# Optimization experiments

Measured on AMD Instinct MI355X. Metric: run time of the kernel, lower is better.

Reference implementation:

```python
import jax, jax.numpy as jnp
import numpy as np

MAX_LEN = 30
CONST_VAL = 0.0

def setup_inputs() -> dict:
    key = jax.random.key(0)
    k1, k2, k3 = jax.random.split(key, 3)
    B, T, F = 131072, 30, 10
    inputs = jax.random.normal(k1, (B, T, F), dtype=jnp.float32)
    w1 = jax.random.normal(k2, (1, MAX_LEN), dtype=jnp.float32) * 0.05
    w2 = jax.random.normal(k3, (1, MAX_LEN), dtype=jnp.float32) * 0.05
    return {"inputs": inputs, "w1": w1, "w2": w2}

def reference(inputs, w1, w2):
    B, T, F = inputs.shape  # T == 30 (hardcoded split count), F < MAX_LEN
    # matmul of (B,1,1) scalar with (1,max_len) == outer product -> (B, max_len)
    r1 = inputs[:, 0, 0][:, None] * w1[0]  # (B, 30)
    r2 = inputs[:, 0, 1][:, None] * w2[0]  # (B, 30)
    # concat along last dim then flatten rows, matching tf concat+reshape(-1,2)
    rc = jnp.stack([r1, r2], axis=-1).reshape(-1, 2)  # (N, 2), N = B*30
    N = rc.shape[0]
    K = (MAX_LEN - F) // 2  # number of shifted copies (original + K-1 shifts)
    # pad K-1 constant rows on top; shift i is rows [K-1-i : K-1-i+N] of padded
    pad = jnp.full((K - 1, 2), CONST_VAL, dtype=jnp.float32)
    P = jnp.concatenate([pad, rc], axis=0)  # (N+K-1, 2)
    shifts = jnp.stack(
        [jax.lax.dynamic_slice_in_dim(P, K - 1 - i, N, axis=0) for i in range(K)],
        axis=1,
    )  # (N, K, 2); shift-major column order matches tf.concat axis=1 order
    tens = shifts.reshape(N, 2 * K)  # (N, 2K)
    # tf.split(30, axis=0) + stack(axis=1): piece j row a = tens[j*B + a]
    tens = tens.reshape(30, B, 2 * K).transpose(1, 0, 2)  # (B, 30, 2K)
    return jnp.concatenate([tens, inputs[:, :, 2:]], axis=2)  # (B, 30, 2K+F-2)
```

## Files before the change

### kernel.cpp

```cpp
#include <hip/hip_runtime.h>


__global__ __launch_bounds__(256) void assign_kernel(
    const float* __restrict__ inp,
    const float* __restrict__ w1,
    const float* __restrict__ w2,
    float* __restrict__ out,
    int B, int nrows) {
    __shared__ float w1s[32], w2s[32];
    int t = threadIdx.x;
    if (t < 30) w1s[t] = w1[t];
    else if (t >= 32 && t < 62) w2s[t - 32] = w2[t - 32];
    __syncthreads();

    int row = blockIdx.x * blockDim.x + t;
    if (row >= nrows) return;

    int b = row / 30;
    int j = row - b * 30;
    int m0 = j * B + b;
    int q0 = m0 / 30;
    int r0 = m0 - q0 * 30;

    float2 xa = *(const float2*)(inp + (size_t)q0 * 300);
    float2 xb = (q0 >= 1) ? *(const float2*)(inp + (size_t)(q0 - 1) * 300)
                          : make_float2(0.f, 0.f);

    float front[20];
#pragma unroll
    for (int i = 0; i < 10; ++i) {
        bool useA = (r0 >= i);
        float2 x = useA ? xa : xb;
        int r = useA ? (r0 - i) : (r0 - i + 30);
        bool valid = useA || (q0 >= 1);
        front[2 * i]     = valid ? x.x * w1s[r] : 0.f;
        front[2 * i + 1] = valid ? x.y * w2s[r] : 0.f;
    }

    const float* tin = inp + (size_t)row * 10 + 2;
    float2 t0 = *(const float2*)(tin + 0);
    float2 t1 = *(const float2*)(tin + 2);
    float2 t2 = *(const float2*)(tin + 4);
    float2 t3 = *(const float2*)(tin + 6);

    float4* o4 = (float4*)(out + (size_t)row * 28);
    o4[0] = make_float4(front[0],  front[1],  front[2],  front[3]);
    o4[1] = make_float4(front[4],  front[5],  front[6],  front[7]);
    o4[2] = make_float4(front[8],  front[9],  front[10], front[11]);
    o4[3] = make_float4(front[12], front[13], front[14], front[15]);
    o4[4] = make_float4(front[16], front[17], front[18], front[19]);
    o4[5] = make_float4(t0.x, t0.y, t1.x, t1.y);
    o4[6] = make_float4(t2.x, t2.y, t3.x, t3.y);
}

extern "C" void kernel_launch(void* const* d_in, const int* in_sizes, int n_in,
                              void* d_out, int out_size, void* d_ws, size_t ws_size,
                              hipStream_t stream) {
    const float* inp = (const float*)d_in[0];
    const float* w1  = (const float*)d_in[1];
    const float* w2  = (const float*)d_in[2];
    float* out = (float*)d_out;

    int B = in_sizes[0] / 300;
    int nrows = B * 30;
    int block = 256;
    int grid = (nrows + block - 1) / block;
    assign_kernel<<<grid, block, 0, stream>>>(inp, w1, w2, out, B, nrows);
}
```

Before: 595.9 us.

## Stage input and output through LDS and precompact scalar pairs into workspace

A small pre-kernel gathers the two leading scalars of every batch item into a compact float2 buffer in workspace, so the main kernel's scattered lookups hit a dense array instead of strided 1200-byte rows. The main kernel loads its tile of input rows into LDS with coalesced float4 reads and builds each 28-float output row in padded shared memory. It then writes the tile back with fully coalesced float4 stores. This adds an extra launch, two barriers and LDS traffic in exchange for better global memory coalescing.

```diff
diff --git a/kernel.cpp b/kernel.cpp
--- a/kernel.cpp
+++ b/kernel.cpp
@@ -1,56 +1,87 @@
 #include <hip/hip_runtime.h>
 
 
-__global__ __launch_bounds__(256) void assign_kernel(
+__global__ __launch_bounds__(256) void pack_kernel(const float* __restrict__ inp,
+                                                   float2* __restrict__ xc, int B) {
+    int q = blockIdx.x * blockDim.x + threadIdx.x;
+    if (q < B) {
+        const float* p = inp + (size_t)q * 300;
+        xc[q] = make_float2(p[0], p[1]);
+    }
+}
+
+#define ROWS 192
+
+__global__ __launch_bounds__(ROWS) void main_kernel(
     const float* __restrict__ inp,
+    const float2* __restrict__ xc,
     const float* __restrict__ w1,
     const float* __restrict__ w2,
     float* __restrict__ out,
     int B, int nrows) {
-    __shared__ float w1s[32], w2s[32];
+    __shared__ float w1s[30], w2s[30];
+    __shared__ float lin[ROWS * 10];
+    __shared__ float lout[ROWS * 29];
+
     int t = threadIdx.x;
+    int base = blockIdx.x * ROWS;
+
     if (t < 30) w1s[t] = w1[t];
     else if (t >= 32 && t < 62) w2s[t - 32] = w2[t - 32];
+
+    {
+        const float4* gin = (const float4*)(inp + (size_t)base * 10);
+        float4* l4 = (float4*)lin;
+        const int nf4 = ROWS * 10 / 4;
+        const int gcap = nrows * 10 / 4;
+#pragma unroll
+        for (int s = 0; s < (nf4 + ROWS - 1) / ROWS; ++s) {
+            int idx = t + ROWS * s;
+            if (idx < nf4 && base * 10 / 4 + idx < gcap) l4[idx] = gin[idx];
+        }
+    }
     __syncthreads();
 
-    int row = blockIdx.x * blockDim.x + t;
-    if (row >= nrows) return;
+    {
+        int row = base + t;
+        if (row >= nrows) row = nrows - 1;
+        int b = row / 30;
+        int j = row - b * 30;
+        int m0 = j * B + b;
+        int q0 = m0 / 30;
+        int r0 = m0 - q0 * 30;
 
-    int b = row / 30;
-    int j = row - b * 30;
-    int m0 = j * B + b;
-    int q0 = m0 / 30;
-    int r0 = m0 - q0 * 30;
+        float2 xa = xc[q0];
+        float2 xb = (q0 >= 1) ? xc[q0 - 1] : make_float2(0.f, 0.f);
 
-    float2 xa = *(const float2*)(inp + (size_t)q0 * 300);
-    float2 xb = (q0 >= 1) ? *(const float2*)(inp + (size_t)(q0 - 1) * 300)
-                          : make_float2(0.f, 0.f);
+        float* lo = lout + t * 29;
+#pragma unroll
+        for (int i = 0; i < 10; ++i) {
+            bool useA = (r0 >= i);
+            float2 x = useA ? xa : xb;
+            int r = useA ? (r0 - i) : (r0 - i + 30);
+            bool valid = useA || (q0 >= 1);
+            lo[2 * i]     = valid ? x.x * w1s[r] : 0.f;
+            lo[2 * i + 1] = valid ? x.y * w2s[r] : 0.f;
+        }
+#pragma unroll
+        for (int u = 0; u < 8; ++u) lo[20 + u] = lin[t * 10 + 2 + u];
+    }
+    __syncthreads();
 
-    float front[20];
+    {
+        float4* gout = (float4*)(out + (size_t)base * 28);
+        const long long gcap = (long long)nrows * 7;
 #pragma unroll
-    for (int i = 0; i < 10; ++i) {
-        bool useA = (r0 >= i);
-        float2 x = useA ? xa : xb;
-        int r = useA ? (r0 - i) : (r0 - i + 30);
-        bool valid = useA || (q0 >= 1);
-        front[2 * i]     = valid ? x.x * w1s[r] : 0.f;
-        front[2 * i + 1] = valid ? x.y * w2s[r] : 0.f;
+        for (int s = 0; s < 7; ++s) {
+            int g = t + ROWS * s;
+            int r = g / 7;
+            int c4 = g - r * 7;
+            const float* lp = lout + r * 29 + c4 * 4;
+            if ((long long)base * 7 + g < gcap)
+                gout[g] = make_float4(lp[0], lp[1], lp[2], lp[3]);
+        }
     }
-
-    const float* tin = inp + (size_t)row * 10 + 2;
-    float2 t0 = *(const float2*)(tin + 0);
-    float2 t1 = *(const float2*)(tin + 2);
-    float2 t2 = *(const float2*)(tin + 4);
-    float2 t3 = *(const float2*)(tin + 6);
-
-    float4* o4 = (float4*)(out + (size_t)row * 28);
-    o4[0] = make_float4(front[0],  front[1],  front[2],  front[3]);
-    o4[1] = make_float4(front[4],  front[5],  front[6],  front[7]);
-    o4[2] = make_float4(front[8],  front[9],  front[10], front[11]);
-    o4[3] = make_float4(front[12], front[13], front[14], front[15]);
-    o4[4] = make_float4(front[16], front[17], front[18], front[19]);
-    o4[5] = make_float4(t0.x, t0.y, t1.x, t1.y);
-    o4[6] = make_float4(t2.x, t2.y, t3.x, t3.y);
 }
 
 extern "C" void kernel_launch(void* const* d_in, const int* in_sizes, int n_in,
@@ -63,7 +94,11 @@
 
     int B = in_sizes[0] / 300;
     int nrows = B * 30;
-    int block = 256;
-    int grid = (nrows + block - 1) / block;
-    assign_kernel<<<grid, block, 0, stream>>>(inp, w1, w2, out, B, nrows);
+
+    float2* xc = (float2*)d_ws;
+
+    pack_kernel<<<(B + 255) / 256, 256, 0, stream>>>(inp, xc, B);
+
+    int grid = (nrows + ROWS - 1) / ROWS;
+    main_kernel<<<grid, ROWS, 0, stream>>>(inp, xc, w1, w2, out, B, nrows);
 }
```

Measured after the change: 557.2 us. 6.5% less time.
